# Optimization experiments

Hardware: AMD Instinct MI355X
Metric: run time of the kernel (lower is better)

The kernel has to match this reference:

```python
import jax, jax.numpy as jnp
import numpy as np

MARGIN = 0.5
EPS = 1e-5
NEG_TOPK = 10  # cfg.XBM.NEG_TOPK; memory path (B != M) uses top-k negatives


def setup_inputs() -> dict:
    key = jax.random.key(0)
    k1, k2, k3, k4 = jax.random.split(key, 4)
    B, M, D, C = 256, 65536, 512, 1000
    inputs_col = jax.random.normal(k1, (B, D), dtype=jnp.float32)
    inputs_row = jax.random.normal(k2, (M, D), dtype=jnp.float32)
    targets_col = jax.random.randint(k3, (B,), 0, C)
    target_row = jax.random.randint(k4, (M,), 0, C)
    return {
        "inputs_col": inputs_col,
        "targets_col": targets_col,
        "inputs_row": inputs_row,
        "target_row": target_row,
    }


def reference(inputs_col, targets_col, inputs_row, target_row):
    # sim_mat: [B, M] dense similarity
    sim = jnp.matmul(inputs_col, inputs_row.T)
    same = targets_col[:, None] == target_row[None, :]  # [B, M]

    # positive pairs: same label and sim < 1 - eps; loss = sum(1 - sim)
    pos_mask = same & (sim < 1.0 - EPS)
    pos_loss = jnp.sum(jnp.where(pos_mask, 1.0 - sim, 0.0), axis=1)  # [B]

    # negative pairs (B != M memory path): top-k largest similarities among
    # different-label entries; loss = sum of those top-k values.
    neg_vals = jnp.where(same, -jnp.inf, sim)  # [B, M]
    topk_vals, _ = jax.lax.top_k(neg_vals, NEG_TOPK)  # [B, k]
    neg_loss = jnp.sum(jnp.where(jnp.isfinite(topk_vals), topk_vals, 0.0), axis=1)

    # loss = sum_i (pos_loss_i + neg_loss_i) / n
    return jnp.mean(pos_loss + neg_loss)
```

## Files before the change

### kernel.cpp

```cpp
#include <hip/hip_runtime.h>
#include <math.h>
#include <float.h>

typedef __attribute__((ext_vector_type(4))) float f32x4;
typedef __attribute__((ext_vector_type(8))) __bf16 bf16x8;
typedef __attribute__((ext_vector_type(4))) __bf16 bf16x4;

#define NEG_TOPK 10
#define BROW 256
#define MT 64
#define BK 64
#define SIMSTR 72
#define BUF 40960

__device__ __forceinline__ void topk_ins(float (&top)[NEG_TOPK], float v) {
    #pragma unroll
    for (int q = NEG_TOPK - 1; q >= 1; --q)
        top[q] = fmaxf(fminf(v, top[q - 1]), top[q]);
    top[0] = fmaxf(top[0], v);
}

__device__ __forceinline__ bf16x4 cvt4(float4 v) {
    bf16x4 r;
    r[0] = (__bf16)v.x; r[1] = (__bf16)v.y;
    r[2] = (__bf16)v.z; r[3] = (__bf16)v.w;
    return r;
}

__global__ __launch_bounds__(512, 2) void cl_pass1(
    const float* __restrict__ A,
    const float* __restrict__ Bm,
    const int* __restrict__ tcol,
    const int* __restrict__ trow,
    float* __restrict__ part_topk,
    float* __restrict__ pos_part,
    int D)
{
    __shared__ char smem[2 * BUF];

    const int mb = blockIdx.x;
    const int j0 = mb * MT;
    const int t  = threadIdx.x;
    const int wave = t >> 6, lane = t & 63;
    const int wr = wave >> 1, wc = wave & 1;
    const int lrow = lane & 15, lk = lane >> 4;

    const float4* A4 = (const float4*)A;
    const float4* B4 = (const float4*)Bm;
    const int ldq = D >> 2;
    const int NSTEP = D / BK;

    const int ra = t >> 4;
    const int k4 = t & 15;
    const int rb = t >> 4;

    f32x4 acc[4][2];
    #pragma unroll
    for (int m = 0; m < 4; ++m)
        #pragma unroll
        for (int n = 0; n < 2; ++n)
            acc[m][n] = (f32x4){0.f, 0.f, 0.f, 0.f};

    float4 ar[8];
    float4 br[2];

    #pragma unroll
    for (int s = 0; s < 8; ++s) ar[s] = A4[(ra + 32 * s) * ldq + k4];
    #pragma unroll
    for (int s = 0; s < 2; ++s) br[s] = B4[(size_t)(j0 + rb + 32 * s) * ldq + k4];
    {
        char* Ab = smem;
        char* Bb = smem + 32768;
        #pragma unroll
        for (int s = 0; s < 8; ++s) {
            int r = ra + 32 * s;
            *(bf16x4*)(Ab + r * 128 + ((k4 * 8) ^ ((r & 7) << 4))) = cvt4(ar[s]);
        }
        #pragma unroll
        for (int s = 0; s < 2; ++s) {
            int r = rb + 32 * s;
            *(bf16x4*)(Bb + r * 128 + ((k4 * 8) ^ ((r & 7) << 4))) = cvt4(br[s]);
        }
    }

    const int swz = (lrow & 7) << 4;

    for (int step = 0; step < NSTEP; ++step) {
        const int cur = step & 1;
        __syncthreads();

        if (step + 1 < NSTEP) {
            const int kq = (step + 1) * (BK / 4);
            #pragma unroll
            for (int s = 0; s < 8; ++s) ar[s] = A4[(ra + 32 * s) * ldq + kq + k4];
            #pragma unroll
            for (int s = 0; s < 2; ++s)
                br[s] = B4[(size_t)(j0 + rb + 32 * s) * ldq + kq + k4];
        }

        {
            const char* Ab = smem + cur * BUF;
            const char* Bb = Ab + 32768;
            #pragma unroll
            for (int ks = 0; ks < 2; ++ks) {
                bf16x8 af[4], bfr[2];
                const int kb = ks * 64 + lk * 16;
                #pragma unroll
                for (int m = 0; m < 4; ++m) {
                    int row = wr * 64 + m * 16 + lrow;
                    af[m] = *(const bf16x8*)(Ab + row * 128 + (kb ^ swz));
                }
                #pragma unroll
                for (int n = 0; n < 2; ++n) {
                    int row = wc * 32 + n * 16 + lrow;
                    bfr[n] = *(const bf16x8*)(Bb + row * 128 + (kb ^ swz));
                }
                #pragma unroll
                for (int m = 0; m < 4; ++m)
                    #pragma unroll
                    for (int n = 0; n < 2; ++n)
                        acc[m][n] = __builtin_amdgcn_mfma_f32_16x16x32_bf16(
                            af[m], bfr[n], acc[m][n], 0, 0, 0);
            }
        }

        if (step + 1 < NSTEP) {
            char* Ab = smem + (cur ^ 1) * BUF;
            char* Bb = Ab + 32768;
            #pragma unroll
            for (int s = 0; s < 8; ++s) {
                int r = ra + 32 * s;
                *(bf16x4*)(Ab + r * 128 + ((k4 * 8) ^ ((r & 7) << 4))) = cvt4(ar[s]);
            }
            #pragma unroll
            for (int s = 0; s < 2; ++s) {
                int r = rb + 32 * s;
                *(bf16x4*)(Bb + r * 128 + ((k4 * 8) ^ ((r & 7) << 4))) = cvt4(br[s]);
            }
        }
    }

    unsigned short* simsb = (unsigned short*)smem;
    #pragma unroll
    for (int m = 0; m < 4; ++m)
        #pragma unroll
        for (int n = 0; n < 2; ++n)
            #pragma unroll
            for (int r = 0; r < 4; ++r) {
                int row = wr * 64 + m * 16 + lk * 4 + r;
                int col = wc * 32 + n * 16 + lrow;
                __bf16 b = (__bf16)acc[m][n][r];
                simsb[row * SIMSTR + col] = *(unsigned short*)&b;
            }
    __syncthreads();

    {
        const int row = t >> 1, half = t & 1;
        const int myc = tcol[row];
        const int4* lab4 = (const int4*)(trow + j0 + half * 32);
        float top[NEG_TOPK];
        #pragma unroll
        for (int q = 0; q < NEG_TOPK; ++q) top[q] = -INFINITY;
        float pos = 0.f;
        #pragma unroll
        for (int j = 0; j < 4; ++j) {
            bf16x8 v8 = *(const bf16x8*)(&simsb[row * SIMSTR + half * 32 + j * 8]);
            int4 l1 = lab4[2 * j], l2 = lab4[2 * j + 1];
            int lab[8] = {l1.x, l1.y, l1.z, l1.w, l2.x, l2.y, l2.z, l2.w};
            #pragma unroll
            for (int e = 0; e < 8; ++e) {
                float s = (float)v8[e];
                bool same = (lab[e] == myc);
                pos += (same && s < 0.99999f) ? (1.f - s) : 0.f;
                topk_ins(top, same ? -INFINITY : s);
            }
        }
        float* mtop = (float*)(smem + BUF);
        float* mpos = (float*)(smem + BUF + 20480);
        #pragma unroll
        for (int q = 0; q < NEG_TOPK; ++q) mtop[t * NEG_TOPK + q] = top[q];
        mpos[t] = pos;
        __syncthreads();
        if (half == 0) {
            const float* ot = &mtop[(t + 1) * NEG_TOPK];
            #pragma unroll
            for (int q = 0; q < NEG_TOPK; ++q) topk_ins(top, ot[q]);
            float post = pos + mpos[t + 1];
            float* dst = part_topk + ((size_t)row * gridDim.x + mb) * NEG_TOPK;
            #pragma unroll
            for (int q = 0; q < NEG_TOPK; ++q) dst[q] = top[q];
            pos_part[(size_t)row * gridDim.x + mb] = post;
        }
    }
}

__global__ __launch_bounds__(256) void cl_pass2(
    const float* __restrict__ part_topk,
    const float* __restrict__ pos_part,
    float* __restrict__ row_tot,
    int nch)
{
    const int i = blockIdx.x;
    const int t = threadIdx.x;
    __shared__ float stop[256][NEG_TOPK];
    __shared__ float stop2[32][NEG_TOPK];
    __shared__ float red[256];

    const int n = nch * NEG_TOPK;
    const float* src = part_topk + (size_t)i * n;
    float top[NEG_TOPK];
    #pragma unroll
    for (int q = 0; q < NEG_TOPK; ++q) top[q] = -INFINITY;
    for (int idx = t; idx < n; idx += 256) topk_ins(top, src[idx]);
    #pragma unroll
    for (int q = 0; q < NEG_TOPK; ++q) stop[t][q] = top[q];

    float pos = 0.0f;
    const float* psrc = pos_part + (size_t)i * nch;
    for (int idx = t; idx < nch; idx += 256) pos += psrc[idx];
    red[t] = pos;
    __syncthreads();

    for (int s2 = 128; s2 >= 1; s2 >>= 1) {
        if (t < s2) red[t] += red[t + s2];
        __syncthreads();
    }

    if (t < 32) {
        float m[NEG_TOPK];
        #pragma unroll
        for (int q = 0; q < NEG_TOPK; ++q) m[q] = -INFINITY;
        for (int l = 0; l < 8; ++l)
            #pragma unroll
            for (int q = 0; q < NEG_TOPK; ++q) topk_ins(m, stop[t * 8 + l][q]);
        #pragma unroll
        for (int q = 0; q < NEG_TOPK; ++q) stop2[t][q] = m[q];
    }
    __syncthreads();

    if (t == 0) {
        float m[NEG_TOPK];
        #pragma unroll
        for (int q = 0; q < NEG_TOPK; ++q) m[q] = -INFINITY;
        for (int l = 0; l < 32; ++l)
            #pragma unroll
            for (int q = 0; q < NEG_TOPK; ++q) topk_ins(m, stop2[l][q]);
        float neg = 0.0f;
        #pragma unroll
        for (int q = 0; q < NEG_TOPK; ++q)
            if (isfinite(m[q])) neg += m[q];
        row_tot[i] = neg + red[0];
    }
}

__global__ __launch_bounds__(256) void cl_pass3(
    const float* __restrict__ row_tot, float* __restrict__ out, int Bn)
{
    __shared__ float red[256];
    const int t = threadIdx.x;
    float v = 0.0f;
    for (int idx = t; idx < Bn; idx += 256) v += row_tot[idx];
    red[t] = v;
    __syncthreads();
    for (int s2 = 128; s2 >= 1; s2 >>= 1) {
        if (t < s2) red[t] += red[t + s2];
        __syncthreads();
    }
    if (t == 0) out[0] = red[0] / (float)Bn;
}

extern "C" void kernel_launch(void* const* d_in, const int* in_sizes, int n_in,
                              void* d_out, int out_size, void* d_ws, size_t ws_size,
                              hipStream_t stream)
{
    const float* A    = (const float*)d_in[0];
    const int*   tcol = (const int*)d_in[1];
    const float* Bm   = (const float*)d_in[2];
    const int*   trow = (const int*)d_in[3];
    float* out = (float*)d_out;

    const int Bn = in_sizes[1];
    const int M  = in_sizes[3];
    const int D  = in_sizes[0] / Bn;
    const int numMB = M / MT;
    const int nch = numMB;

    float* part_topk = (float*)d_ws;
    float* pos_part  = part_topk + (size_t)Bn * nch * NEG_TOPK;
    float* row_tot   = pos_part + (size_t)Bn * nch;

    cl_pass1<<<numMB, 512, 0, stream>>>(A, Bm, tcol, trow, part_topk, pos_part, D);
    cl_pass2<<<Bn, 256, 0, stream>>>(part_topk, pos_part, row_tot, nch);
    cl_pass3<<<1, 256, 0, stream>>>(row_tot, out, Bn);
}
```

Before: 260.2 us.

## Pre-convert A to swizzled bf16 and stream it into LDS via global_load_lds

```diff
diff --git a/kernel.cpp b/kernel.cpp
--- a/kernel.cpp
+++ b/kernel.cpp
@@ -11,6 +11,7 @@
 #define MT 64
 #define BK 64
 #define SIMSTR 72
+#define ABYTES 32768
 #define BUF 40960
 
 __device__ __forceinline__ void topk_ins(float (&top)[NEG_TOPK], float v) {
@@ -27,8 +28,22 @@
     return r;
 }
 
+__global__ __launch_bounds__(256) void cl_pass0(
+    const float* __restrict__ A, char* __restrict__ A_swz, int D)
+{
+    const int idx = blockIdx.x * 256 + threadIdx.x;
+    const int r    = idx >> 7;
+    const int rem  = idx & 127;
+    const int step = rem >> 4;
+    const int g    = rem & 15;
+    float4 v = ((const float4*)A)[r * (D >> 2) + rem];
+    bf16x4 b = cvt4(v);
+    const int off = step * ABYTES + r * 128 + ((g * 8) ^ ((r & 7) << 4));
+    *(unsigned long long*)(A_swz + off) = *(unsigned long long*)&b;
+}
+
 __global__ __launch_bounds__(512, 2) void cl_pass1(
-    const float* __restrict__ A,
+    const char* __restrict__ A_swz,
     const float* __restrict__ Bm,
     const int* __restrict__ tcol,
     const int* __restrict__ trow,
@@ -45,14 +60,12 @@
     const int wr = wave >> 1, wc = wave & 1;
     const int lrow = lane & 15, lk = lane >> 4;
 
-    const float4* A4 = (const float4*)A;
     const float4* B4 = (const float4*)Bm;
     const int ldq = D >> 2;
     const int NSTEP = D / BK;
 
-    const int ra = t >> 4;
+    const int rb = t >> 4;
     const int k4 = t & 15;
-    const int rb = t >> 4;
 
     f32x4 acc[4][2];
     #pragma unroll
@@ -61,25 +74,29 @@
         for (int n = 0; n < 2; ++n)
             acc[m][n] = (f32x4){0.f, 0.f, 0.f, 0.f};
 
-    float4 ar[8];
-    float4 br[2];
-
-    #pragma unroll
-    for (int s = 0; s < 8; ++s) ar[s] = A4[(ra + 32 * s) * ldq + k4];
-    #pragma unroll
-    for (int s = 0; s < 2; ++s) br[s] = B4[(size_t)(j0 + rb + 32 * s) * ldq + k4];
+    float4 brA[2], brB[2];
+
+    const char* gA = A_swz + wave * 4096 + lane * 16;
+    char* lA0 = smem + wave * 4096;
+    char* lA1 = smem + BUF + wave * 4096;
+
+    #pragma unroll
+    for (int q = 0; q < 4; ++q)
+        __builtin_amdgcn_global_load_lds(
+            (const __attribute__((address_space(1))) void*)(gA + q * 1024),
+            (__attribute__((address_space(3))) void*)(lA0 + q * 1024), 16, 0, 0);
+    #pragma unroll
+    for (int s = 0; s < 2; ++s)
+        brA[s] = B4[(size_t)(j0 + rb + 32 * s) * ldq + 0 * (BK / 4) + k4];
+    #pragma unroll
+    for (int s = 0; s < 2; ++s)
+        brB[s] = B4[(size_t)(j0 + rb + 32 * s) * ldq + 1 * (BK / 4) + k4];
     {
-        char* Ab = smem;
-        char* Bb = smem + 32768;
-        #pragma unroll
-        for (int s = 0; s < 8; ++s) {
-            int r = ra + 32 * s;
-            *(bf16x4*)(Ab + r * 128 + ((k4 * 8) ^ ((r & 7) << 4))) = cvt4(ar[s]);
-        }
+        char* Bb = smem + ABYTES;
         #pragma unroll
         for (int s = 0; s < 2; ++s) {
             int r = rb + 32 * s;
-            *(bf16x4*)(Bb + r * 128 + ((k4 * 8) ^ ((r & 7) << 4))) = cvt4(br[s]);
+            *(bf16x4*)(Bb + r * 128 + ((k4 * 8) ^ ((r & 7) << 4))) = cvt4(brA[s]);
         }
     }
 
@@ -87,20 +104,29 @@
 
     for (int step = 0; step < NSTEP; ++step) {
         const int cur = step & 1;
-        __syncthreads();
+        asm volatile("s_waitcnt vmcnt(0) lgkmcnt(0)" ::: "memory");
+        __builtin_amdgcn_s_barrier();
 
         if (step + 1 < NSTEP) {
-            const int kq = (step + 1) * (BK / 4);
-            #pragma unroll
-            for (int s = 0; s < 8; ++s) ar[s] = A4[(ra + 32 * s) * ldq + kq + k4];
+            const char* gp = gA + (step + 1) * ABYTES;
+            char* lp = cur ? lA0 : lA1;
+            #pragma unroll
+            for (int q = 0; q < 4; ++q)
+                __builtin_amdgcn_global_load_lds(
+                    (const __attribute__((address_space(1))) void*)(gp + q * 1024),
+                    (__attribute__((address_space(3))) void*)(lp + q * 1024), 16, 0, 0);
+        }
+        if (step + 2 < NSTEP) {
+            const int kq = (step + 2) * (BK / 4);
+            float4* dst = (step & 1) ? brB : brA;
             #pragma unroll
             for (int s = 0; s < 2; ++s)
-                br[s] = B4[(size_t)(j0 + rb + 32 * s) * ldq + kq + k4];
+                dst[s] = B4[(size_t)(j0 + rb + 32 * s) * ldq + kq + k4];
         }
 
         {
             const char* Ab = smem + cur * BUF;
-            const char* Bb = Ab + 32768;
+            const char* Bb = Ab + ABYTES;
             #pragma unroll
             for (int ks = 0; ks < 2; ++ks) {
                 bf16x8 af[4], bfr[2];
@@ -125,17 +151,12 @@
         }
 
         if (step + 1 < NSTEP) {
-            char* Ab = smem + (cur ^ 1) * BUF;
-            char* Bb = Ab + 32768;
-            #pragma unroll
-            for (int s = 0; s < 8; ++s) {
-                int r = ra + 32 * s;
-                *(bf16x4*)(Ab + r * 128 + ((k4 * 8) ^ ((r & 7) << 4))) = cvt4(ar[s]);
-            }
+            char* Bb = smem + (cur ^ 1) * BUF + ABYTES;
+            const float4* src = (step & 1) ? brA : brB;
             #pragma unroll
             for (int s = 0; s < 2; ++s) {
                 int r = rb + 32 * s;
-                *(bf16x4*)(Bb + r * 128 + ((k4 * 8) ^ ((r & 7) << 4))) = cvt4(br[s]);
+                *(bf16x4*)(Bb + r * 128 + ((k4 * 8) ^ ((r & 7) << 4))) = cvt4(src[s]);
             }
         }
     }
@@ -285,11 +306,14 @@
     const int numMB = M / MT;
     const int nch = numMB;
 
-    float* part_topk = (float*)d_ws;
+    char* A_swz = (char*)d_ws;
+    float* part_topk = (float*)(A_swz + 8 * ABYTES);
     float* pos_part  = part_topk + (size_t)Bn * nch * NEG_TOPK;
     float* row_tot   = pos_part + (size_t)Bn * nch;
 
-    cl_pass1<<<numMB, 512, 0, stream>>>(A, Bm, tcol, trow, part_topk, pos_part, D);
+    cl_pass0<<<128, 256, 0, stream>>>(A, A_swz, D);
+    cl_pass1<<<numMB, 512, 0, stream>>>(A_swz, Bm, tcol, trow,
+                                        part_topk, pos_part, D);
     cl_pass2<<<Bn, 256, 0, stream>>>(part_topk, pos_part, row_tot, nch);
     cl_pass3<<<1, 256, 0, stream>>>(row_tot, out, Bn);
 }
```

Result: slower. 294.8 us (+13.3%).
